# Kernel tuning notes

Hardware: AMD Instinct MI355X
Metric: run time of the kernel (lower is better)

Reference implementation:

```python
import jax, jax.numpy as jnp
import numpy as np

N = 6144      # nodes
IN = 512      # input_dim
D = 256       # HIDDEN_DIM (out_features per head)
H = 1         # HEADS
OUT = 128     # OUT_DIM
ALPHA = 0.2   # LeakyReLU slope
EPS = 1e-5    # LayerNorm eps


def _xavier(k, shape):
    fan_in, fan_out = shape[-2], shape[-1]
    lim = float(np.sqrt(6.0 / (fan_in + fan_out)))
    return jax.random.uniform(k, shape, jnp.float32, -lim, lim)


def _gat(x, W, a_src, a_dst, adj):
    # x: [N, IN], W: [IN, H*D], a_src/a_dst: [H, D], adj: [N, N] int
    n = x.shape[0]
    h = (x @ W).reshape(n, H, D)                       # [N, H, D]
    e1 = jnp.einsum('nhd,hd->nh', h, a_src)            # src score
    e2 = jnp.einsum('nhd,hd->nh', h, a_dst)            # dst score
    e = jax.nn.leaky_relu(e1[:, None, :] + e2[None, :, :], ALPHA)  # [N, N, H]
    e = jnp.where(adj[:, :, None] > 0, e, jnp.float32(-1e9))
    att = jnp.nan_to_num(jax.nn.softmax(e, axis=1), nan=0.0)       # softmax over dim -2 (j)
    out = jnp.einsum('nbh,bhd->nhd', att, h)           # weighted aggregation over j
    return out.reshape(n, H * D)                       # is_concat=True


def _ln(x, g, b):
    m = jnp.mean(x, axis=-1, keepdims=True)
    v = jnp.mean((x - m) ** 2, axis=-1, keepdims=True)
    return (x - m) * jax.lax.rsqrt(v + EPS) * g + b


def setup_inputs() -> dict:
    key = jax.random.key(0)
    ks = jax.random.split(key, 20)
    inp = {
        'x': jax.random.normal(ks[0], (N, IN), jnp.float32),
        'adj_cf': jax.random.randint(ks[1], (N, N), 0, 2, jnp.int32),
        'adj_org': jax.random.randint(ks[2], (N, N), 0, 2, jnp.int32),
        'adj_per': jax.random.randint(ks[3], (N, N), 0, 2, jnp.int32),
        'W_cf': _xavier(ks[4], (IN, H * D)),
        'a_src_cf': _xavier(ks[5], (H, D)),
        'a_dst_cf': _xavier(ks[6], (H, D)),
        'W_org': _xavier(ks[7], (IN, H * D)),
        'a_src_org': _xavier(ks[8], (H, D)),
        'a_dst_org': _xavier(ks[9], (H, D)),
        'W_per': _xavier(ks[10], (IN, H * D)),
        'a_src_per': _xavier(ks[11], (H, D)),
        'a_dst_per': _xavier(ks[12], (H, D)),
        'proj_W': _xavier(ks[13], (H * D, OUT)),
        'proj_b': jnp.zeros((OUT,), jnp.float32),
        'ln_g': jnp.ones((OUT,), jnp.float32),
        'ln_b': jnp.zeros((OUT,), jnp.float32),
        'alpha': jnp.ones((3, 1), jnp.float32),
    }
    return inp


def reference(x, adj_cf, adj_org, adj_per,
              W_cf, a_src_cf, a_dst_cf,
              W_org, a_src_org, a_dst_org,
              W_per, a_src_per, a_dst_per,
              proj_W, proj_b, ln_g, ln_b, alpha):
    # dropout layers are identity in eval mode
    h_cf = _gat(x, W_cf, a_src_cf, a_dst_cf, adj_cf)
    h_org = _gat(x, W_org, a_src_org, a_dst_org, adj_org)
    h_per = _gat(x, W_per, a_src_per, a_dst_per, adj_per)
    z_cf = _ln(h_cf @ proj_W + proj_b, ln_g, ln_b)
    z_org = _ln(h_org @ proj_W + proj_b, ln_g, ln_b)
    z_per = _ln(h_per @ proj_W + proj_b, ln_g, ln_b)
    w = jax.nn.softmax(alpha, axis=0)                  # [3, 1]
    z = w[0] * z_cf + w[1] * z_org + w[2] * z_per
    z = jnp.nan_to_num(z, nan=0.0, posinf=0.0, neginf=0.0)
    return (z, w)
```

## Files before the change

### kernel.cpp

```cpp
#include <hip/hip_runtime.h>

typedef _Float16 half_t;
typedef _Float16 f16x8 __attribute__((ext_vector_type(8)));
typedef _Float16 f16x4 __attribute__((ext_vector_type(4)));
typedef float f32x4 __attribute__((ext_vector_type(4)));
typedef unsigned long long u64;

#define NN 6144
#define IN_DIM 512
#define DD 256
#define OUT_DIM 128
#define SPLIT 4
#define JT 24
#define LOG2E 1.44269504088896340736f

__device__ __forceinline__ f32x4 mfma16(f16x8 a, f16x8 b, f32x4 c) {
  return __builtin_amdgcn_mfma_f32_16x16x32_f16(a, b, c, 0, 0, 0);
}

__device__ __forceinline__ unsigned enc_f(float f) {
  unsigned b = __float_as_uint(f);
  return (b & 0x80000000u) ? ~b : (b | 0x80000000u);
}
__device__ __forceinline__ float dec_f(unsigned u) {
  return (u & 0x80000000u) ? __uint_as_float(u & 0x7fffffffu)
                           : __uint_as_float(~u);
}

__global__ void cvt_kernel(const float* __restrict__ x,
                           const float* __restrict__ W0, const float* __restrict__ W1,
                           const float* __restrict__ W2, const float* __restrict__ pW,
                           half_t* __restrict__ xh, half_t* __restrict__ WT,
                           half_t* __restrict__ pWT, unsigned* __restrict__ e2mu) {
  int bx = blockIdx.x, t = threadIdx.x;
  if (bx < 3072) {
    int idx = (bx * 256 + t) * 4;
    float4 v = *(const float4*)(x + idx);
    f16x4 h;
    h[0] = (half_t)v.x; h[1] = (half_t)v.y; h[2] = (half_t)v.z; h[3] = (half_t)v.w;
    *(f16x4*)(xh + idx) = h;
    return;
  }
  int idx2 = bx - 3072;
  if (idx2 == 0 && t < 3) e2mu[t] = 0x00800000u;
  int y = idx2 >> 9;
  int idx = ((idx2 & 511) << 8) + t;
  if (y < 3) {
    const float* W = (y == 0) ? W0 : (y == 1) ? W1 : W2;
    int k = idx >> 8, n = idx & 255;
    WT[(size_t)y * DD * IN_DIM + (size_t)n * IN_DIM + k] = (half_t)W[idx];
  } else if (idx < DD * OUT_DIM) {
    int k = idx >> 7, o = idx & 127;
    pWT[(size_t)o * DD + k] = (half_t)pW[idx];
  }
}

__global__ __launch_bounds__(256, 2) void gemm1_kernel(
    const half_t* __restrict__ xh, const half_t* __restrict__ WT,
    const float* __restrict__ as0, const float* __restrict__ as1, const float* __restrict__ as2,
    const float* __restrict__ ad0, const float* __restrict__ ad1, const float* __restrict__ ad2,
    half_t* __restrict__ hT, float* __restrict__ e1, float* __restrict__ e2,
    unsigned* __restrict__ e2mu) {
  int v = blockIdx.y;
  int i0 = blockIdx.x * 64;
  int t = threadIdx.x;
  int lane = t & 63, w = t >> 6;
  int lr = lane & 15, lg = lane >> 4;
  const half_t* Wv = WT + (size_t)v * DD * IN_DIM;
  const float* asv = (v == 0) ? as0 : (v == 1) ? as1 : as2;
  const float* adv = (v == 0) ? ad0 : (v == 1) ? ad1 : ad2;
  f32x4 acc[4][4] = {};
  for (int kt = 0; kt < 16; ++kt) {
    int k = kt * 32 + lg * 8;
    f16x8 af[4], bf[4];
#pragma unroll
    for (int mf = 0; mf < 4; ++mf)
      af[mf] = *(const f16x8*)(xh + (size_t)(i0 + mf * 16 + lr) * IN_DIM + k);
#pragma unroll
    for (int nf = 0; nf < 4; ++nf)
      bf[nf] = *(const f16x8*)(Wv + (size_t)(w * 64 + nf * 16 + lr) * IN_DIM + k);
#pragma unroll
    for (int mf = 0; mf < 4; ++mf)
#pragma unroll
      for (int nf = 0; nf < 4; ++nf)
        acc[mf][nf] = mfma16(af[mf], bf[nf], acc[mf][nf]);
  }
  __shared__ half_t tr[4][64 * 64];
  __shared__ float ep1[4][64], ep2[4][64];
  char* trw = (char*)tr[w];
#pragma unroll
  for (int mf = 0; mf < 4; ++mf)
#pragma unroll
    for (int nf = 0; nf < 4; ++nf)
#pragma unroll
      for (int r = 0; r < 4; ++r) {
        int dl = nf * 16 + lr;
        int il = mf * 16 + lg * 4 + r;
        unsigned addr = (unsigned)((dl * 128 + il * 2) ^ ((dl & 7) << 4));
        *(half_t*)(trw + addr) = (half_t)acc[mf][nf][r];
      }
  float as_c[4], ad_c[4];
#pragma unroll
  for (int nf = 0; nf < 4; ++nf) {
    int col = w * 64 + nf * 16 + lr;
    as_c[nf] = asv[col];
    ad_c[nf] = adv[col];
  }
#pragma unroll
  for (int mf = 0; mf < 4; ++mf)
#pragma unroll
    for (int r = 0; r < 4; ++r) {
      float p1 = 0.f, p2 = 0.f;
#pragma unroll
      for (int nf = 0; nf < 4; ++nf) {
        p1 = fmaf(acc[mf][nf][r], as_c[nf], p1);
        p2 = fmaf(acc[mf][nf][r], ad_c[nf], p2);
      }
      p1 += __shfl_xor(p1, 1); p1 += __shfl_xor(p1, 2);
      p1 += __shfl_xor(p1, 4); p1 += __shfl_xor(p1, 8);
      p2 += __shfl_xor(p2, 1); p2 += __shfl_xor(p2, 2);
      p2 += __shfl_xor(p2, 4); p2 += __shfl_xor(p2, 8);
      if (lr == 0) {
        int il = mf * 16 + lg * 4 + r;
        ep1[w][il] = p1;
        ep2[w][il] = p2;
      }
    }
  __syncthreads();
  half_t* hTv = hT + (size_t)v * DD * NN;
#pragma unroll
  for (int c = 0; c < 8; ++c) {
    unsigned addr = (unsigned)((lane * 128 + c * 16) ^ ((lane & 7) << 4));
    f16x8 val = *(const f16x8*)(trw + addr);
    *(f16x8*)(hTv + (size_t)(w * 64 + lane) * NN + i0 + c * 8) = val;
  }
  if (t < 64) {
    float e1v = LOG2E * (ep1[0][t] + ep1[1][t] + ep1[2][t] + ep1[3][t]);
    float e2v = LOG2E * (ep2[0][t] + ep2[1][t] + ep2[2][t] + ep2[3][t]);
    e1[v * NN + i0 + t] = e1v;
    e2[v * NN + i0 + t] = e2v;
    float m = e2v;
    m = fmaxf(m, __shfl_xor(m, 1));  m = fmaxf(m, __shfl_xor(m, 2));
    m = fmaxf(m, __shfl_xor(m, 4));  m = fmaxf(m, __shfl_xor(m, 8));
    m = fmaxf(m, __shfl_xor(m, 16)); m = fmaxf(m, __shfl_xor(m, 32));
    if (t == 0) atomicMax(e2mu + v, enc_f(m));
  }
}

__global__ __launch_bounds__(256, 2) void gat_kernel(
    const int* __restrict__ adj0, const int* __restrict__ adj1, const int* __restrict__ adj2,
    const half_t* __restrict__ hT,
    const float* __restrict__ e1g, const float* __restrict__ e2g,
    const unsigned* __restrict__ e2mu, half_t* __restrict__ pacc, float* __restrict__ pl) {
  int v = blockIdx.z, s = blockIdx.y;
  const int* __restrict__ adjv = (v == 0) ? adj0 : (v == 1) ? adj1 : adj2;
  int i0 = blockIdx.x * 64;
  int t = threadIdx.x;
  int lane = t & 63, w = t >> 6;
  int lr = lane & 15, lg = lane >> 4;
  int jq = t & 15, rg = t >> 4;

  __shared__ half_t hbuf0[DD * 64];
  __shared__ half_t hbuf1[DD * 64];
  __shared__ half_t P0[64 * 64];
  __shared__ half_t P1[64 * 64];

  const half_t* hTv = hT + (size_t)v * DD * NN;
  const float* e2v = e2g + v * NN;
  const int jbase = s * JT * 64;

  float e1r[4], mr[4];
  float e2mL = dec_f(e2mu[v]);
#pragma unroll
  for (int it = 0; it < 4; ++it) {
    float e1i = e1g[v * NN + i0 + it * 16 + rg];
    e1r[it] = e1i;
    float sm = e1i + e2mL;
    mr[it] = fmaxf(sm, 0.2f * sm);
  }

  f32x4 acc[4][4] = {};
  float lpart[4] = {0.f, 0.f, 0.f, 0.f};

  int sub = lane >> 3;
  int c_src = (lane & 7) ^ sub;
  auto gload = [&](half_t* hb, int jt) {
    int j0 = jbase + jt * 64;
#pragma unroll
    for (int q = 0; q < 8; ++q) {
      const half_t* gp = hTv + (size_t)(w * 64 + q * 8 + sub) * NN + j0 + c_src * 8;
      half_t* lp = hb + (w * 8 + q) * 512;
      __builtin_amdgcn_global_load_lds(
          (const __attribute__((address_space(1))) int*)gp,
          (__attribute__((address_space(3))) int*)lp, 16, 0, 0);
    }
  };
  auto load_adj = [&](int4 (&aw)[4], int jt) {
    int j0 = jbase + jt * 64;
#pragma unroll
    for (int it = 0; it < 4; ++it)
      aw[it] = *(const int4*)(adjv + (size_t)(i0 + it * 16 + rg) * NN + j0 + jq * 4);
  };
  auto comp_p = [&](const int4 (&aw)[4], const float4& e2q, char* pb) {
    float e2a[4] = {e2q.x, e2q.y, e2q.z, e2q.w};
#pragma unroll
    for (int it = 0; it < 4; ++it) {
      int il = it * 16 + rg;
      int a4[4] = {aw[it].x, aw[it].y, aw[it].z, aw[it].w};
      f16x4 ph;
      float ssum = 0.f;
#pragma unroll
      for (int c = 0; c < 4; ++c) {
        float s1 = e1r[it] + e2a[c];
        float u = fmaxf(s1, 0.2f * s1) - mr[it];
        float p = (a4[c] > 0) ? exp2f(u) : 0.f;
        ssum += p;
        ph[c] = (half_t)p;
      }
      lpart[it] += ssum;
      unsigned addr = (unsigned)((il * 128 + jq * 8) ^ ((il & 7) << 4));
      *(f16x4*)(pb + addr) = ph;
    }
  };
  auto do_mfma = [&](const char* pb, const half_t* hb) {
    __builtin_amdgcn_s_setprio(1);
#pragma unroll
    for (int kf = 0; kf < 2; ++kf) {
      f16x8 bfr[4];
#pragma unroll
      for (int nf = 0; nf < 4; ++nf) {
        int d = w * 64 + nf * 16 + lr;
        unsigned ba = (unsigned)(d * 128 + ((kf * 64 + lg * 16) ^ ((lr & 7) << 4)));
        bfr[nf] = *(const f16x8*)((const char*)hb + ba);
      }
#pragma unroll
      for (int mf = 0; mf < 4; ++mf) {
        int row = mf * 16 + lr;
        unsigned pa_ = (unsigned)((row * 128 + kf * 64 + lg * 16) ^ ((row & 7) << 4));
        f16x8 af = *(const f16x8*)(pb + pa_);
#pragma unroll
        for (int nf = 0; nf < 4; ++nf)
          acc[mf][nf] = mfma16(af, bfr[nf], acc[mf][nf]);
      }
    }
    __builtin_amdgcn_s_setprio(0);
  };

  int4 awA[4], awB[4];
  float4 e2A, e2B;

  load_adj(awA, 0);
  e2A = *(const float4*)(e2v + jbase + jq * 4);
  gload(hbuf0, 0);
  __syncthreads();

  for (int tt = 0; tt < JT; tt += 2) {
    comp_p(awA, e2A, (char*)P0);
    __syncthreads();
    {
      load_adj(awB, tt + 1);
      e2B = *(const float4*)(e2v + jbase + (tt + 1) * 64 + jq * 4);
      gload(hbuf1, tt + 1);
    }
    do_mfma((char*)P0, hbuf0);

    comp_p(awB, e2B, (char*)P1);
    __syncthreads();
    if (tt + 2 < JT) {
      load_adj(awA, tt + 2);
      e2A = *(const float4*)(e2v + jbase + (tt + 2) * 64 + jq * 4);
      gload(hbuf0, tt + 2);
    }
    do_mfma((char*)P1, hbuf1);
  }

  size_t sl = (size_t)v * SPLIT + s;
#pragma unroll
  for (int it = 0; it < 4; ++it) {
    float ssum = lpart[it];
    ssum += __shfl_xor(ssum, 1); ssum += __shfl_xor(ssum, 2);
    ssum += __shfl_xor(ssum, 4); ssum += __shfl_xor(ssum, 8);
    if (jq == 0) pl[sl * NN + i0 + it * 16 + rg] = ssum;
  }

  half_t* pa = pacc + sl * (size_t)NN * DD;
#pragma unroll
  for (int mf = 0; mf < 4; ++mf)
#pragma unroll
    for (int r = 0; r < 4; ++r) {
      int il = mf * 16 + lg * 4 + r;
#pragma unroll
      for (int nf = 0; nf < 4; ++nf)
        pa[(size_t)(i0 + il) * DD + w * 64 + nf * 16 + lr] = (half_t)acc[mf][nf][r];
    }
}

__global__ __launch_bounds__(64) void proj_kernel(
    const half_t* __restrict__ pacc, const float* __restrict__ pl,
    const half_t* __restrict__ pWT,
    const float* __restrict__ proj_b, const float* __restrict__ ln_g,
    const float* __restrict__ ln_b, const float* __restrict__ alpha,
    float* __restrict__ out) {
  int i0 = blockIdx.x * 16;
  int t = threadIdx.x;
  int lr = t & 15, lg = t >> 4;
  float a0 = alpha[0], a1 = alpha[1], a2 = alpha[2];
  float am = fmaxf(a0, fmaxf(a1, a2));
  float x0 = __expf(a0 - am), x1 = __expf(a1 - am), x2 = __expf(a2 - am);
  float inv = 1.f / (x0 + x1 + x2);
  float wv[3] = {x0 * inv, x1 * inv, x2 * inv};
  __shared__ float rlv[3][16];
  if (t < 48) {
    int v = t >> 4, i = t & 15;
    float l = 0.f;
#pragma unroll
    for (int s = 0; s < SPLIT; ++s)
      l += pl[((size_t)v * SPLIT + s) * NN + i0 + i];
    rlv[v][i] = (l > 0.f) ? 1.f / l : 0.f;
  }
  float pb[8], gg[8], bb[8];
#pragma unroll
  for (int nf = 0; nf < 8; ++nf) {
    pb[nf] = proj_b[nf * 16 + lr];
    gg[nf] = ln_g[nf * 16 + lr];
    bb[nf] = ln_b[nf * 16 + lr];
  }
  __syncthreads();
  f32x4 zacc[8] = {};
  for (int v = 0; v < 3; ++v) {
    float rl = rlv[v][lr];
    f32x4 yac[8] = {};
    const half_t* p0 = pacc + (((size_t)v * SPLIT + 0) * NN + i0 + lr) * DD;
    const half_t* p1 = pacc + (((size_t)v * SPLIT + 1) * NN + i0 + lr) * DD;
    const half_t* p2 = pacc + (((size_t)v * SPLIT + 2) * NN + i0 + lr) * DD;
    const half_t* p3 = pacc + (((size_t)v * SPLIT + 3) * NN + i0 + lr) * DD;
    for (int kt = 0; kt < 8; ++kt) {
      int k = kt * 32 + lg * 8;
      f16x8 s0 = *(const f16x8*)(p0 + k);
      f16x8 s1 = *(const f16x8*)(p1 + k);
      f16x8 s2 = *(const f16x8*)(p2 + k);
      f16x8 s3 = *(const f16x8*)(p3 + k);
      f16x8 af;
#pragma unroll
      for (int e = 0; e < 8; ++e)
        af[e] = (half_t)((((float)s0[e] + (float)s1[e]) +
                          ((float)s2[e] + (float)s3[e])) * rl);
#pragma unroll
      for (int nf = 0; nf < 8; ++nf) {
        f16x8 bf = *(const f16x8*)(pWT + (size_t)(nf * 16 + lr) * DD + k);
        yac[nf] = mfma16(af, bf, yac[nf]);
      }
    }
#pragma unroll
    for (int r = 0; r < 4; ++r) {
      float ssum = 0.f, q = 0.f;
#pragma unroll
      for (int nf = 0; nf < 8; ++nf) {
        float y = yac[nf][r] + pb[nf];
        yac[nf][r] = y;
        ssum += y; q += y * y;
      }
      ssum += __shfl_xor(ssum, 1); ssum += __shfl_xor(ssum, 2);
      ssum += __shfl_xor(ssum, 4); ssum += __shfl_xor(ssum, 8);
      q += __shfl_xor(q, 1); q += __shfl_xor(q, 2);
      q += __shfl_xor(q, 4); q += __shfl_xor(q, 8);
      float mean = ssum * (1.f / 128.f);
      float var = q * (1.f / 128.f) - mean * mean;
      float rstd = rsqrtf(var + 1e-5f);
      float wvv = wv[v];
#pragma unroll
      for (int nf = 0; nf < 8; ++nf)
        zacc[nf][r] += wvv * (yac[nf][r] - mean) * rstd;
    }
  }
#pragma unroll
  for (int nf = 0; nf < 8; ++nf)
#pragma unroll
    for (int r = 0; r < 4; ++r) {
      int row = i0 + lg * 4 + r;
      float z = zacc[nf][r] * gg[nf] + bb[nf];
      if (!isfinite(z)) z = 0.f;
      out[(size_t)row * OUT_DIM + nf * 16 + lr] = z;
    }
  if (blockIdx.x == 0 && t < 3) out[(size_t)NN * OUT_DIM + t] = wv[t];
}

extern "C" void kernel_launch(void* const* d_in, const int* in_sizes, int n_in,
                              void* d_out, int out_size, void* d_ws, size_t ws_size,
                              hipStream_t stream) {
  const float* x      = (const float*)d_in[0];
  const int*   adj_cf = (const int*)d_in[1];
  const int*   adj_or = (const int*)d_in[2];
  const int*   adj_pe = (const int*)d_in[3];
  const float* W_cf   = (const float*)d_in[4];
  const float* as_cf  = (const float*)d_in[5];
  const float* ad_cf  = (const float*)d_in[6];
  const float* W_or   = (const float*)d_in[7];
  const float* as_or  = (const float*)d_in[8];
  const float* ad_or  = (const float*)d_in[9];
  const float* W_pe   = (const float*)d_in[10];
  const float* as_pe  = (const float*)d_in[11];
  const float* ad_pe  = (const float*)d_in[12];
  const float* proj_W = (const float*)d_in[13];
  const float* proj_b = (const float*)d_in[14];
  const float* ln_g   = (const float*)d_in[15];
  const float* ln_b   = (const float*)d_in[16];
  const float* alpha  = (const float*)d_in[17];

  char* ws = (char*)d_ws;
  half_t*   xh     = (half_t*)(ws + 0);
  half_t*   WT     = (half_t*)(ws + 6291456);
  half_t*   pWT    = (half_t*)(ws + 7077888);
  half_t*   hT     = (half_t*)(ws + 7143424);
  float*    e1     = (float*)(ws + 16580608);
  float*    e2     = (float*)(ws + 16654336);
  unsigned* e2mu   = (unsigned*)(ws + 16728064);
  half_t*   pacc   = (half_t*)(ws + 16728128);
  float*    pl     = (float*)(ws + 54476864);

  cvt_kernel<<<5120, 256, 0, stream>>>(x, W_cf, W_or, W_pe, proj_W, xh, WT, pWT, e2mu);
  gemm1_kernel<<<dim3(96, 3), 256, 0, stream>>>(xh, WT, as_cf, as_or, as_pe,
                                                ad_cf, ad_or, ad_pe, hT, e1, e2, e2mu);
  gat_kernel<<<dim3(96, SPLIT, 3), 256, 0, stream>>>(adj_cf, adj_or, adj_pe, hT,
                                                     e1, e2, e2mu, pacc, pl);
  proj_kernel<<<384, 64, 0, stream>>>(pacc, pl, pWT, proj_b, ln_g, ln_b, alpha,
                                      (float*)d_out);
}
```

Measured before the change: 241.8 us.

## Deepen GAT aggregation pipeline with manual waitcnt barriers and prefetch two tiles ahead

Restructures the attention-aggregation main loop so that adjacency and e2 loads are issued two tiles ahead while the h tile is loaded one tile ahead. __syncthreads is replaced with a barrier that waits only on LDS counters, plus an explicit partial vmcnt wait and sched_barrier fences to pin the instruction order. The aim is to keep global loads in flight across the MFMA phase instead of draining them at every barrier. The hand-counted vmcnt(5) is only correct if the number of outstanding loads issued matches that count, which makes the code fragile.

```diff
diff --git a/kernel.cpp b/kernel.cpp
--- a/kernel.cpp
+++ b/kernel.cpp
@@ -17,6 +17,10 @@
 __device__ __forceinline__ f32x4 mfma16(f16x8 a, f16x8 b, f32x4 c) {
   return __builtin_amdgcn_mfma_f32_16x16x32_f16(a, b, c, 0, 0, 0);
 }
+
+#define LBAR() asm volatile("s_waitcnt lgkmcnt(0)\n\ts_barrier" ::: "memory")
+#define VWAIT(N) asm volatile("s_waitcnt vmcnt(" #N ")")
+#define SBAR() __builtin_amdgcn_sched_barrier(0)
 
 __device__ __forceinline__ unsigned enc_f(float f) {
   unsigned b = __float_as_uint(f);
@@ -251,28 +255,51 @@
 
   load_adj(awA, 0);
   e2A = *(const float4*)(e2v + jbase + jq * 4);
+  SBAR();
   gload(hbuf0, 0);
-  __syncthreads();
-
-  for (int tt = 0; tt < JT; tt += 2) {
+  SBAR();
+  load_adj(awB, 1);
+  e2B = *(const float4*)(e2v + jbase + 64 + jq * 4);
+  SBAR();
+
+#define REGION_F(T, AWc, E2c, Pc, Hc, Hn)                            \
+  {                                                                  \
+    comp_p(AWc, E2c, (char*)(Pc));                                   \
+    LBAR();                                                          \
+    SBAR();                                                          \
+    VWAIT(5);                                                        \
+    SBAR();                                                          \
+    gload(Hn, (T) + 1);                                              \
+    SBAR();                                                          \
+    load_adj(AWc, (T) + 2);                                          \
+    E2c = *(const float4*)(e2v + jbase + ((T) + 2) * 64 + jq * 4);   \
+    SBAR();                                                          \
+    do_mfma((char*)(Pc), Hc);                                        \
+  }
+
+  for (int tt = 0; tt < JT - 2; tt += 2) {
+    REGION_F(tt,     awA, e2A, P0, hbuf0, hbuf1);
+    REGION_F(tt + 1, awB, e2B, P1, hbuf1, hbuf0);
+  }
+  {
     comp_p(awA, e2A, (char*)P0);
-    __syncthreads();
-    {
-      load_adj(awB, tt + 1);
-      e2B = *(const float4*)(e2v + jbase + (tt + 1) * 64 + jq * 4);
-      gload(hbuf1, tt + 1);
-    }
+    LBAR();
+    SBAR();
+    VWAIT(5);
+    SBAR();
+    gload(hbuf1, JT - 1);
+    SBAR();
     do_mfma((char*)P0, hbuf0);
-
+  }
+  {
     comp_p(awB, e2B, (char*)P1);
-    __syncthreads();
-    if (tt + 2 < JT) {
-      load_adj(awA, tt + 2);
-      e2A = *(const float4*)(e2v + jbase + (tt + 2) * 64 + jq * 4);
-      gload(hbuf0, tt + 2);
-    }
+    LBAR();
+    SBAR();
+    VWAIT(0);
+    SBAR();
     do_mfma((char*)P1, hbuf1);
   }
+#undef REGION_F
 
   size_t sl = (size_t)v * SPLIT + s;
 #pragma unroll
```

After: 238.5 us. Within noise of the previous version (-1.4%).

## Read hT B-fragments directly from global, widen j-tile to 128, halve split

Applied to the files above, without the earlier changes.

The GAT aggregation kernel no longer stages hT tiles into LDS through global_load_lds. Each wave now loads its MFMA B fragments straight from global memory, and LDS holds only the probability tiles, which grow to 64x128 with a 16-row XOR swizzle. The j-tile widens to 128 and the split-K factor drops from 4 to 2, which halves the partial accumulators written and read by the projection kernel. Barriers become lightweight lgkmcnt waits plus s_barrier, and adjacency is prefetched two tiles ahead. In exchange the hT data is no longer shared across waves through LDS, so there is more redundant global/L2 traffic, and the grid has half as many blocks.

```diff
diff --git a/kernel.cpp b/kernel.cpp
--- a/kernel.cpp
+++ b/kernel.cpp
@@ -10,13 +10,15 @@
 #define IN_DIM 512
 #define DD 256
 #define OUT_DIM 128
-#define SPLIT 4
+#define SPLIT 2
 #define JT 24
 #define LOG2E 1.44269504088896340736f
 
 __device__ __forceinline__ f32x4 mfma16(f16x8 a, f16x8 b, f32x4 c) {
   return __builtin_amdgcn_mfma_f32_16x16x32_f16(a, b, c, 0, 0, 0);
 }
+
+#define LBAR() asm volatile("s_waitcnt lgkmcnt(0)\n\ts_barrier" ::: "memory")
 
 __device__ __forceinline__ unsigned enc_f(float f) {
   unsigned b = __float_as_uint(f);
@@ -160,14 +162,12 @@
   int lr = lane & 15, lg = lane >> 4;
   int jq = t & 15, rg = t >> 4;
 
-  __shared__ half_t hbuf0[DD * 64];
-  __shared__ half_t hbuf1[DD * 64];
-  __shared__ half_t P0[64 * 64];
-  __shared__ half_t P1[64 * 64];
+  __shared__ half_t P0[64 * 128];
+  __shared__ half_t P1[64 * 128];
 
   const half_t* hTv = hT + (size_t)v * DD * NN;
   const float* e2v = e2g + v * NN;
-  const int jbase = s * JT * 64;
+  const int jbase = s * JT * 128;
 
   float e1r[4], mr[4];
   float e2mL = dec_f(e2mu[v]);
@@ -182,61 +182,58 @@
   f32x4 acc[4][4] = {};
   float lpart[4] = {0.f, 0.f, 0.f, 0.f};
 
-  int sub = lane >> 3;
-  int c_src = (lane & 7) ^ sub;
-  auto gload = [&](half_t* hb, int jt) {
-    int j0 = jbase + jt * 64;
-#pragma unroll
-    for (int q = 0; q < 8; ++q) {
-      const half_t* gp = hTv + (size_t)(w * 64 + q * 8 + sub) * NN + j0 + c_src * 8;
-      half_t* lp = hb + (w * 8 + q) * 512;
-      __builtin_amdgcn_global_load_lds(
-          (const __attribute__((address_space(1))) int*)gp,
-          (__attribute__((address_space(3))) int*)lp, 16, 0, 0);
+  auto load_adj = [&](int4 (&aw)[4][2], int jt) {
+    int j0 = jbase + jt * 128;
+#pragma unroll
+    for (int it = 0; it < 4; ++it) {
+      const int* ap = adjv + (size_t)(i0 + it * 16 + rg) * NN + j0 + jq * 4;
+      aw[it][0] = *(const int4*)ap;
+      aw[it][1] = *(const int4*)(ap + 64);
     }
   };
-  auto load_adj = [&](int4 (&aw)[4], int jt) {
-    int j0 = jbase + jt * 64;
-#pragma unroll
-    for (int it = 0; it < 4; ++it)
-      aw[it] = *(const int4*)(adjv + (size_t)(i0 + it * 16 + rg) * NN + j0 + jq * 4);
+  auto load_e2 = [&](float4 (&e2q)[2], int jt) {
+    int j0 = jbase + jt * 128;
+    e2q[0] = *(const float4*)(e2v + j0 + jq * 4);
+    e2q[1] = *(const float4*)(e2v + j0 + 64 + jq * 4);
   };
-  auto comp_p = [&](const int4 (&aw)[4], const float4& e2q, char* pb) {
-    float e2a[4] = {e2q.x, e2q.y, e2q.z, e2q.w};
-#pragma unroll
-    for (int it = 0; it < 4; ++it) {
-      int il = it * 16 + rg;
-      int a4[4] = {aw[it].x, aw[it].y, aw[it].z, aw[it].w};
-      f16x4 ph;
-      float ssum = 0.f;
-#pragma unroll
-      for (int c = 0; c < 4; ++c) {
-        float s1 = e1r[it] + e2a[c];
-        float u = fmaxf(s1, 0.2f * s1) - mr[it];
-        float p = (a4[c] > 0) ? exp2f(u) : 0.f;
-        ssum += p;
-        ph[c] = (half_t)p;
-      }
-      lpart[it] += ssum;
-      unsigned addr = (unsigned)((il * 128 + jq * 8) ^ ((il & 7) << 4));
-      *(f16x4*)(pb + addr) = ph;
+  auto comp_p = [&](const int4 (&aw)[4][2], const float4 (&e2q)[2], char* pb) {
+#pragma unroll
+    for (int jp = 0; jp < 2; ++jp) {
+      float e2a[4] = {e2q[jp].x, e2q[jp].y, e2q[jp].z, e2q[jp].w};
+#pragma unroll
+      for (int it = 0; it < 4; ++it) {
+        int il = it * 16 + rg;
+        int a4[4] = {aw[it][jp].x, aw[it][jp].y, aw[it][jp].z, aw[it][jp].w};
+        f16x4 ph;
+        float ssum = 0.f;
+#pragma unroll
+        for (int c = 0; c < 4; ++c) {
+          float s1 = e1r[it] + e2a[c];
+          float u = fmaxf(s1, 0.2f * s1) - mr[it];
+          float p = (a4[c] > 0) ? exp2f(u) : 0.f;
+          ssum += p;
+          ph[c] = (half_t)p;
+        }
+        lpart[it] += ssum;
+        unsigned addr = (unsigned)(il * 256 + ((jp * 128 + jq * 8) ^ ((il & 15) << 4)));
+        *(f16x4*)(pb + addr) = ph;
+      }
     }
   };
-  auto do_mfma = [&](const char* pb, const half_t* hb) {
+  auto do_mfma = [&](const char* pb, int jt) {
+    int j0 = jbase + jt * 128;
     __builtin_amdgcn_s_setprio(1);
 #pragma unroll
-    for (int kf = 0; kf < 2; ++kf) {
+    for (int kf = 0; kf < 4; ++kf) {
       f16x8 bfr[4];
 #pragma unroll
-      for (int nf = 0; nf < 4; ++nf) {
-        int d = w * 64 + nf * 16 + lr;
-        unsigned ba = (unsigned)(d * 128 + ((kf * 64 + lg * 16) ^ ((lr & 7) << 4)));
-        bfr[nf] = *(const f16x8*)((const char*)hb + ba);
-      }
+      for (int nf = 0; nf < 4; ++nf)
+        bfr[nf] = *(const f16x8*)(hTv + (size_t)(w * 64 + nf * 16 + lr) * NN +
+                                  j0 + kf * 32 + lg * 8);
 #pragma unroll
       for (int mf = 0; mf < 4; ++mf) {
         int row = mf * 16 + lr;
-        unsigned pa_ = (unsigned)((row * 128 + kf * 64 + lg * 16) ^ ((row & 7) << 4));
+        unsigned pa_ = (unsigned)(row * 256 + ((kf * 64 + lg * 16) ^ ((row & 15) << 4)));
         f16x8 af = *(const f16x8*)(pb + pa_);
 #pragma unroll
         for (int nf = 0; nf < 4; ++nf)
@@ -246,32 +243,21 @@
     __builtin_amdgcn_s_setprio(0);
   };
 
-  int4 awA[4], awB[4];
-  float4 e2A, e2B;
-
-  load_adj(awA, 0);
-  e2A = *(const float4*)(e2v + jbase + jq * 4);
-  gload(hbuf0, 0);
-  __syncthreads();
+  int4 awA[4][2], awB[4][2];
+  float4 e2A[2], e2B[2];
+
+  load_adj(awA, 0); load_e2(e2A, 0);
+  load_adj(awB, 1); load_e2(e2B, 1);
 
   for (int tt = 0; tt < JT; tt += 2) {
     comp_p(awA, e2A, (char*)P0);
-    __syncthreads();
-    {
-      load_adj(awB, tt + 1);
-      e2B = *(const float4*)(e2v + jbase + (tt + 1) * 64 + jq * 4);
-      gload(hbuf1, tt + 1);
-    }
-    do_mfma((char*)P0, hbuf0);
-
+    LBAR();
+    if (tt + 2 < JT) { load_adj(awA, tt + 2); load_e2(e2A, tt + 2); }
+    do_mfma((char*)P0, tt);
     comp_p(awB, e2B, (char*)P1);
-    __syncthreads();
-    if (tt + 2 < JT) {
-      load_adj(awA, tt + 2);
-      e2A = *(const float4*)(e2v + jbase + (tt + 2) * 64 + jq * 4);
-      gload(hbuf0, tt + 2);
-    }
-    do_mfma((char*)P1, hbuf1);
+    LBAR();
+    if (tt + 3 < JT) { load_adj(awB, tt + 3); load_e2(e2B, tt + 3); }
+    do_mfma((char*)P1, tt + 1);
   }
 
   size_t sl = (size_t)v * SPLIT + s;
@@ -312,10 +298,8 @@
   __shared__ float rlv[3][16];
   if (t < 48) {
     int v = t >> 4, i = t & 15;
-    float l = 0.f;
-#pragma unroll
-    for (int s = 0; s < SPLIT; ++s)
-      l += pl[((size_t)v * SPLIT + s) * NN + i0 + i];
+    float l = pl[((size_t)v * SPLIT + 0) * NN + i0 + i] +
+              pl[((size_t)v * SPLIT + 1) * NN + i0 + i];
     rlv[v][i] = (l > 0.f) ? 1.f / l : 0.f;
   }
   float pb[8], gg[8], bb[8];
@@ -332,19 +316,14 @@
     f32x4 yac[8] = {};
     const half_t* p0 = pacc + (((size_t)v * SPLIT + 0) * NN + i0 + lr) * DD;
     const half_t* p1 = pacc + (((size_t)v * SPLIT + 1) * NN + i0 + lr) * DD;
-    const half_t* p2 = pacc + (((size_t)v * SPLIT + 2) * NN + i0 + lr) * DD;
-    const half_t* p3 = pacc + (((size_t)v * SPLIT + 3) * NN + i0 + lr) * DD;
     for (int kt = 0; kt < 8; ++kt) {
       int k = kt * 32 + lg * 8;
       f16x8 s0 = *(const f16x8*)(p0 + k);
       f16x8 s1 = *(const f16x8*)(p1 + k);
-      f16x8 s2 = *(const f16x8*)(p2 + k);
-      f16x8 s3 = *(const f16x8*)(p3 + k);
       f16x8 af;
 #pragma unroll
       for (int e = 0; e < 8; ++e)
-        af[e] = (half_t)((((float)s0[e] + (float)s1[e]) +
-                          ((float)s2[e] + (float)s3[e])) * rl);
+        af[e] = (half_t)(((float)s0[e] + (float)s1[e]) * rl);
 #pragma unroll
       for (int nf = 0; nf < 8; ++nf) {
         f16x8 bf = *(const f16x8*)(pWT + (size_t)(nf * 16 + lr) * DD + k);
@@ -416,7 +395,7 @@
   float*    e2     = (float*)(ws + 16654336);
   unsigned* e2mu   = (unsigned*)(ws + 16728064);
   half_t*   pacc   = (half_t*)(ws + 16728128);
-  float*    pl     = (float*)(ws + 54476864);
+  float*    pl     = (float*)(ws + 35602496);
 
   cvt_kernel<<<5120, 256, 0, stream>>>(x, W_cf, W_or, W_pe, proj_W, xh, WT, pWT, e2mu);
   gemm1_kernel<<<dim3(96, 3), 256, 0, stream>>>(xh, WT, as_cf, as_or, as_pe,
```

Result: slower. 375.5 us (+55.3%).
